# Performance work log

Measured on AMD Instinct MI355X. Metric: run time of the kernel, lower is better.

## Reference

```python
import jax, jax.numpy as jnp
import numpy as np

N_E = 8192
E_DIM = 256
BETA = 0.25
DECAY = 0.99
EPSILON = 1e-05


def setup_inputs() -> dict:
    key = jax.random.key(0)
    k1, k2 = jax.random.split(key)
    z = jax.random.normal(k1, (16, 2048, E_DIM), dtype=jnp.float32)
    # xavier_uniform for [n_e, e_dim]
    bound = float(np.sqrt(6.0 / (N_E + E_DIM)))
    embeddings = jax.random.uniform(k2, (N_E, E_DIM), dtype=jnp.float32,
                                    minval=-bound, maxval=bound)
    return {"z": z, "embeddings": embeddings}


def reference(z, embeddings):
    old_shape = z.shape
    z_flat = z.reshape(-1, E_DIM)  # [N, D]

    # squared-distance: ||z||^2 + ||e||^2 - 2 z.e  -> [N, n_e]
    distances = (jnp.sum(z_flat * z_flat, axis=1, keepdims=True)
                 + jnp.sum(embeddings * embeddings, axis=1)
                 - 2.0 * jnp.einsum('nd,kd->nk', z_flat, embeddings))
    idx = jnp.argmin(distances, axis=1)  # [N] int

    z_q = embeddings[idx].reshape(old_shape)

    # --- EMA codebook update (training, first step: counter 0 -> 1,
    # hidden starts at 0 so the bias-corrected average equals the value) ---
    ones = jnp.ones_like(idx, dtype=jnp.float32)
    bins = jax.ops.segment_sum(ones, idx, num_segments=N_E)          # [n_e]
    dw = jax.ops.segment_sum(z_flat, idx, num_segments=N_E)          # [n_e, D]
    ema_cluster = bins   # EMA step 1 with zero-init hidden == value
    ema_dw = dw
    n = jnp.sum(ema_cluster)
    cluster = (ema_cluster + EPSILON) / (n + N_E * EPSILON) * n
    new_embeddings = ema_dw / cluster[:, None]

    loss = BETA * jnp.mean((z - jax.lax.stop_gradient(z_q)) ** 2)
    z_q_st = z + jax.lax.stop_gradient(z_q - z)  # straight-through
    return z_q_st, idx, loss, new_embeddings
```

## Files before the change

kernel.cpp:

```cpp
#include <hip/hip_runtime.h>
#include <math.h>
#include <float.h>

#define N_ROWS 32768
#define EDIM 256
#define NE 8192
#define NTILES 64
#define DELTA 1.6e-3f
#define RB 8

typedef unsigned int uint32;
typedef unsigned long long uint64;
typedef __attribute__((ext_vector_type(8))) _Float16 f16x8;
typedef __attribute__((ext_vector_type(4))) float f32x4;

#define OFF_ZCAT    ((size_t)0)
#define OFF_ECAT    ((size_t)33554432)
#define OFF_ET      ((size_t)37748736)
#define OFF_EN      ((size_t)46268416)
#define OFF_PV      ((size_t)46301184)
#define OFF_PI      ((size_t)54689792)
#define OFF_PV2     ((size_t)63078400)
#define OFF_IDX     ((size_t)71467008)
#define OFF_BINS    ((size_t)71598080)
#define OFF_PACKED  ((size_t)71630848)
#define OFF_FLAGCNT ((size_t)71892992)
#define OFF_FLAGGED ((size_t)71893504)

__device__ __forceinline__ uint32 pack2_f16(float a, float b) {
    _Float16 ha = (_Float16)a;
    _Float16 hb = (_Float16)b;
    unsigned short ua = __builtin_bit_cast(unsigned short, ha);
    unsigned short ub = __builtin_bit_cast(unsigned short, hb);
    return (uint32)ua | ((uint32)ub << 16);
}

__device__ __forceinline__ void gload_lds16(const void* g, void* l) {
    __builtin_amdgcn_global_load_lds(
        (const __attribute__((address_space(1))) uint32*)g,
        (__attribute__((address_space(3))) uint32*)l, 16, 0, 0);
}

__device__ __forceinline__ float np_pairwise_sumsq(const float* a) {
#pragma clang fp contract(off)
    float h0, h1;
    #pragma unroll 1
    for (int hb = 0; hb < 2; ++hb) {
        const float* p = a + hb * 128;
        float r0=p[0]*p[0], r1=p[1]*p[1], r2=p[2]*p[2], r3=p[3]*p[3],
              r4=p[4]*p[4], r5=p[5]*p[5], r6=p[6]*p[6], r7=p[7]*p[7];
        #pragma unroll 1
        for (int i = 8; i < 128; i += 8) {
            r0 += p[i+0]*p[i+0]; r1 += p[i+1]*p[i+1];
            r2 += p[i+2]*p[i+2]; r3 += p[i+3]*p[i+3];
            r4 += p[i+4]*p[i+4]; r5 += p[i+5]*p[i+5];
            r6 += p[i+6]*p[i+6]; r7 += p[i+7]*p[i+7];
        }
        float s = ((r0+r1)+(r2+r3))+((r4+r5)+(r6+r7));
        if (hb == 0) h0 = s; else h1 = s;
    }
    return h0 + h1;
}

__global__ void k_prep(const float* __restrict__ Z, const float* __restrict__ E,
                       unsigned short* __restrict__ Zcat, unsigned short* __restrict__ Ecat,
                       float* __restrict__ ET, float* __restrict__ en,
                       uint64* __restrict__ packed, int* __restrict__ hist,
                       int* __restrict__ flagcnt) {
    __shared__ float tile[8][264];
    int b = blockIdx.x;
    int t = threadIdx.x;
    if (b < 4096) {
        int r = b * 8 + (t >> 5);
        int u = t & 31;
        int c = u >> 2, q = u & 3;
        int lq = q ^ ((r >> 1) & 3);
        int k0 = c * 32 + lq * 8;
        const float4* zp = (const float4*)(Z + (size_t)r * EDIM + k0);
        float4 a = zp[0], bb = zp[1];
        float f[8] = {a.x,a.y,a.z,a.w,bb.x,bb.y,bb.z,bb.w};
        uint32 o[4];
        #pragma unroll
        for (int j = 0; j < 4; ++j) o[j] = pack2_f16(f[2*j], f[2*j+1]);
        *(uint4*)(Zcat + (size_t)r * 256 + c * 32 + q * 8) = make_uint4(o[0],o[1],o[2],o[3]);
    } else if (b < 5120) {
        int eb = b - 4096;
        int r8 = t >> 5;
        int r = eb * 8 + r8;
        int u = t & 31;
        int c = u >> 2, q = u & 3;
        int lq = q ^ ((r >> 1) & 3);
        int k0 = c * 32 + lq * 8;
        const float4* ep = (const float4*)(E + (size_t)r * EDIM + k0);
        float4 a = ep[0], bb = ep[1];
        float f[8] = {a.x,a.y,a.z,a.w,bb.x,bb.y,bb.z,bb.w};
        uint32 o[4];
        #pragma unroll
        for (int j = 0; j < 4; ++j) o[j] = pack2_f16(256.0f*f[2*j], 256.0f*f[2*j+1]);
        *(uint4*)(Ecat + (size_t)r * 256 + c * 32 + q * 8) = make_uint4(o[0],o[1],o[2],o[3]);
        *(float4*)&tile[r8][k0]     = make_float4(f[0], f[1], f[2], f[3]);
        *(float4*)&tile[r8][k0 + 4] = make_float4(f[4], f[5], f[6], f[7]);
        __syncthreads();
        float4 lo, hi;
        lo.x = tile[0][t]; lo.y = tile[1][t]; lo.z = tile[2][t]; lo.w = tile[3][t];
        hi.x = tile[4][t]; hi.y = tile[5][t]; hi.z = tile[6][t]; hi.w = tile[7][t];
        float* dst = ET + (size_t)t * NE + eb * 8;
        *(float4*)dst = lo;
        *(float4*)(dst + 4) = hi;
    } else if (b < 5152) {
        int k = (b - 5120) * 256 + t;
        en[k] = np_pairwise_sumsq(E + (size_t)k * EDIM);
    } else if (b < 5184) {
        int i = (b - 5152) * 256 + t;
        #pragma unroll
        for (int j = 0; j < 4; ++j) packed[i + j*8192] = 0xFFFFFFFFFFFFFFFFull;
    } else {
        hist[(b - 5184) * 256 + t] = 0;
        if (b == 5184 && t == 0) *flagcnt = 0;
    }
}

__device__ __forceinline__ uint32 float_key(float v) {
    uint32 b = __float_as_uint(v);
    return (b & 0x80000000u) ? ~b : (b | 0x80000000u);
}

__global__ __launch_bounds__(256, 4) void k_gemm(
    const unsigned short* __restrict__ Zcat, const unsigned short* __restrict__ Ecat,
    const float* __restrict__ enorm,
    float* __restrict__ pv, int* __restrict__ pi, float* __restrict__ pv2)
{
    __shared__ __align__(16) char UB[33024];
    __shared__ float ens[128];
    __shared__ float fv1[128]; __shared__ int fi1[128]; __shared__ float fv2[128];

    unsigned short* As0 = (unsigned short*)(UB);
    unsigned short* As1 = (unsigned short*)(UB + 8192);
    unsigned short* Bs0 = (unsigned short*)(UB + 16384);
    unsigned short* Bs1 = (unsigned short*)(UB + 24576);

    int t = threadIdx.x;
    int nt = blockIdx.x & 63, mt = blockIdx.x >> 6;
    int wid = t >> 6, lane = t & 63;
    int wmg = wid >> 1, wng = wid & 1;
    int wm = wmg * 64, wn = wng * 64;

    if (t < 128) ens[t] = enorm[nt*128 + t];

    int j0 = wid*2, j1 = j0 + 1;
    int r0 = j0*16 + (lane >> 2), r1 = j1*16 + (lane >> 2);
    int c8 = (lane & 3) * 8;
    const unsigned short* gA0 = Zcat + (size_t)(mt*128 + r0)*256 + c8;
    const unsigned short* gA1 = Zcat + (size_t)(mt*128 + r1)*256 + c8;
    const unsigned short* gB0 = Ecat + (size_t)(nt*128 + r0)*256 + c8;
    const unsigned short* gB1 = Ecat + (size_t)(nt*128 + r1)*256 + c8;
    unsigned short* lA0s0 = As0 + j0*512;  unsigned short* lA1s0 = As0 + j1*512;
    unsigned short* lA0s1 = As1 + j0*512;  unsigned short* lA1s1 = As1 + j1*512;
    unsigned short* lB0s0 = Bs0 + j0*512;  unsigned short* lB1s0 = Bs0 + j1*512;
    unsigned short* lB0s1 = Bs1 + j0*512;  unsigned short* lB1s1 = Bs1 + j1*512;

    f32x4 acc[4][4];
    #pragma unroll
    for (int i = 0; i < 4; ++i)
        #pragma unroll
        for (int j = 0; j < 4; ++j) acc[i][j] = (f32x4){0.f,0.f,0.f,0.f};

    int frow = lane & 15, q = lane >> 4;
    int sw = (frow >> 1) & 3;
    const unsigned short* a0Base = As0 + (wm + frow)*32 + ((q ^ sw) * 8);
    const unsigned short* a1Base = As1 + (wm + frow)*32 + ((q ^ sw) * 8);
    const unsigned short* b0Base = Bs0 + (wn + frow)*32 + ((q ^ sw) * 8);
    const unsigned short* b1Base = Bs1 + (wn + frow)*32 + ((q ^ sw) * 8);

    gload_lds16(gA0, lA0s0);
    gload_lds16(gA1, lA1s0);
    gload_lds16(gB0, lB0s0);
    gload_lds16(gB1, lB1s0);
    __syncthreads();

    #pragma unroll 1
    for (int c = 0; c < 8; ++c) {
        int nxt = c + 1;
        if (nxt < 8) {
            int aOff = nxt * 32;
            if (nxt & 1) {
                gload_lds16(gA0 + aOff, lA0s1);
                gload_lds16(gA1 + aOff, lA1s1);
                gload_lds16(gB0 + aOff, lB0s1);
                gload_lds16(gB1 + aOff, lB1s1);
            } else {
                gload_lds16(gA0 + aOff, lA0s0);
                gload_lds16(gA1 + aOff, lA1s0);
                gload_lds16(gB0 + aOff, lB0s0);
                gload_lds16(gB1 + aOff, lB1s0);
            }
        }
        const unsigned short* aB = (c & 1) ? a1Base : a0Base;
        const unsigned short* bB = (c & 1) ? b1Base : b0Base;
        f16x8 af[4], bfr[4];
        #pragma unroll
        for (int i = 0; i < 4; ++i) bfr[i] = *(const f16x8*)(bB + i*16*32);
        #pragma unroll
        for (int i = 0; i < 4; ++i) af[i] = *(const f16x8*)(aB + i*16*32);
        #pragma unroll
        for (int i = 0; i < 4; ++i)
            #pragma unroll
            for (int j = 0; j < 4; ++j)
                acc[i][j] = __builtin_amdgcn_mfma_f32_16x16x32_f16(af[i], bfr[j], acc[i][j], 0, 0, 0);
        __syncthreads();
    }

    float ensr[4]; int nn[4];
    #pragma unroll
    for (int j = 0; j < 4; ++j) {
        int nl = wn + j*16 + frow;
        nn[j] = nt*128 + nl;
        ensr[j] = ens[nl];
    }
    uint4* P = (uint4*)UB;
    int gbase = wng*64 + wmg*32 + q*4;

    #pragma unroll
    for (int ih = 0; ih < 2; ++ih) {
        #pragma unroll
        for (int i2 = 0; i2 < 2; ++i2) {
            int i = ih*2 + i2;
            #pragma unroll
            for (int r = 0; r < 4; ++r) {
                float s0 = fmaf(-0.0078125f, acc[i][0][r], ensr[0]);
                float s1 = fmaf(-0.0078125f, acc[i][1][r], ensr[1]);
                float s2 = fmaf(-0.0078125f, acc[i][2][r], ensr[2]);
                float s3 = fmaf(-0.0078125f, acc[i][3][r], ensr[3]);
                float v1 = s0; int i1 = nn[0];
                float v2 = fmaxf(v1, s1);
                if (s1 < v1) i1 = nn[1];
                v1 = fminf(v1, s1);
                v2 = fminf(v2, fmaxf(v1, s2));
                if (s2 < v1) i1 = nn[2];
                v1 = fminf(v1, s2);
                v2 = fminf(v2, fmaxf(v1, s3));
                if (s3 < v1) i1 = nn[3];
                v1 = fminf(v1, s3);
                P[frow*129 + gbase + i2*16 + r] =
                    make_uint4(__float_as_uint(v1), (uint32)i1, __float_as_uint(v2), 0u);
            }
        }
        __syncthreads();
        if (t < 128) {
            const uint4* base = P + t;
            uint4 e0 = base[0];
            float v1 = __uint_as_float(e0.x); int i1 = (int)e0.y;
            float v2 = __uint_as_float(e0.z);
            #pragma unroll
            for (int f = 1; f < 16; ++f) {
                uint4 e = base[f*129];
                float ov1 = __uint_as_float(e.x), ov2 = __uint_as_float(e.z);
                v2 = fminf(fminf(v2, ov2), fmaxf(v1, ov1));
                if (ov1 < v1) i1 = (int)e.y;
                v1 = fminf(v1, ov1);
            }
            fv1[t] = v1; fi1[t] = i1; fv2[t] = v2;
        }
        __syncthreads();
        if (t < 64) {
            float v1 = fv1[t], v2 = fv2[t]; int i1 = fi1[t];
            float ov1 = fv1[64+t], ov2 = fv2[64+t];
            v2 = fminf(fminf(v2, ov2), fmaxf(v1, ov1));
            if (ov1 < v1) i1 = fi1[64+t];
            v1 = fminf(v1, ov1);
            size_t o = (size_t)nt * N_ROWS + mt*128 + (t>>5)*64 + ih*32 + (t&31);
            pv[o] = v1; pi[o] = i1; pv2[o] = v2;
        }
    }
}

__global__ void k_merge(const float* __restrict__ pv, const int* __restrict__ pi,
                        const float* __restrict__ pv2,
                        float* __restrict__ out_idx_f, int* __restrict__ idxint,
                        int* __restrict__ flagcnt, int* __restrict__ flagged) {
    int g = blockIdx.x * 256 + threadIdx.x;
    float B1 = FLT_MAX, B2 = FLT_MAX; int I1 = 0;
    #pragma unroll 1
    for (int p = 0; p < NTILES; ++p) {
        size_t o = (size_t)p * N_ROWS + g;
        float v1 = pv[o], v2 = pv2[o]; int i1 = pi[o];
        if (v1 < B1) { B2 = fminf(B1, v2); B1 = v1; I1 = i1; }
        else B2 = fminf(B2, v1);
    }
    out_idx_f[g] = (float)I1;
    idxint[g] = I1;
    if (B2 - B1 < DELTA) {
        int slot = atomicAdd(flagcnt, 1);
        flagged[slot] = g;
    }
}

__global__ void k_phaseB(const float* __restrict__ Z, const float* __restrict__ ET,
                         const float* __restrict__ enorm,
                         const int* __restrict__ flagcnt, const int* __restrict__ flagged,
                         uint64* __restrict__ packed) {
    __shared__ float zl[RB][256];
    __shared__ float znl[RB];
    __shared__ int rows[RB];
    __shared__ float sv[256]; __shared__ int si[256];
    int t = threadIdx.x;
    int cnt = *flagcnt; if (cnt > N_ROWS) cnt = N_ROWS;
    int ngrp = (cnt + RB - 1) / RB;
    int ntask = ngrp * 8;
    #pragma unroll 1
    for (int task = blockIdx.x; task < ntask; task += gridDim.x) {
        int slice = task & 7;
        int g0 = (task >> 3) * RB;
        __syncthreads();
        if (t < RB) {
            int f = g0 + t;
            rows[t] = flagged[f < cnt ? f : g0];
        }
        __syncthreads();
        #pragma unroll
        for (int rr = 0; rr < RB; ++rr) zl[rr][t] = Z[(size_t)rows[rr]*EDIM + t];
        __syncthreads();
        if (t < RB) znl[t] = np_pairwise_sumsq(&zl[t][0]);
        __syncthreads();

        float acc[RB][4];
        #pragma unroll
        for (int rr = 0; rr < RB; ++rr)
            #pragma unroll
            for (int c = 0; c < 4; ++c) acc[rr][c] = 0.f;
        const float* eb = ET + slice*1024 + t;
        #pragma unroll 1
        for (int d = 0; d < 256; ++d) {
            const float* ep = eb + (size_t)d * NE;
            float v0 = ep[0], v1 = ep[256], v2 = ep[512], v3 = ep[768];
            #pragma unroll
            for (int rr = 0; rr < RB; ++rr) {
                float zd = zl[rr][d];
                acc[rr][0] = fmaf(zd, v0, acc[rr][0]);
                acc[rr][1] = fmaf(zd, v1, acc[rr][1]);
                acc[rr][2] = fmaf(zd, v2, acc[rr][2]);
                acc[rr][3] = fmaf(zd, v3, acc[rr][3]);
            }
        }
        #pragma unroll 1
        for (int rr = 0; rr < RB; ++rr) {
            int row = rows[rr];
            float zn = znl[rr];
            float bv = FLT_MAX; int bi = 0x7fffffff;
            {
#pragma clang fp contract(off)
                #pragma unroll
                for (int c = 0; c < 4; ++c) {
                    int k = slice*1024 + c*256 + t;
                    float S  = zn + enorm[k];
                    float tw = 2.0f * acc[rr][c];
                    float sc = S - tw;
                    if (sc < bv || (sc == bv && k < bi)) { bv = sc; bi = k; }
                }
            }
            sv[t] = bv; si[t] = bi;
            __syncthreads();
            for (int st = 128; st > 0; st >>= 1) {
                if (t < st) {
                    float ov = sv[t+st]; int oi = si[t+st];
                    if (ov < sv[t] || (ov == sv[t] && oi < si[t])) { sv[t] = ov; si[t] = oi; }
                }
                __syncthreads();
            }
            if (t == 0) {
                uint64 pk = ((uint64)float_key(sv[0]) << 32) | (uint32)si[0];
                atomicMin(packed + row, pk);
            }
            __syncthreads();
        }
    }
}

__global__ void k_taila(const float* __restrict__ Z, const float* __restrict__ E,
                        int* __restrict__ idxint, const uint64* __restrict__ packed,
                        float* __restrict__ out0, float* __restrict__ out_idx_f,
                        int* __restrict__ hist, float* __restrict__ lossp) {
    __shared__ float wsum[4];
    int t = threadIdx.x;
    int w = t >> 6, lane = t & 63;
    int row = blockIdx.x * 4 + w;
    int idx = idxint[row];
    uint64 pk = packed[row];
    if (pk != 0xFFFFFFFFFFFFFFFFull) {
        idx = (int)(uint32)(pk & 0xffffffffu);
        if (lane == 0) { out_idx_f[row] = (float)idx; idxint[row] = idx; }
    }
    float4 z4 = ((const float4*)Z)[(size_t)row * 64 + lane];
    float4 e4 = ((const float4*)E)[(size_t)idx * 64 + lane];
    float4 d4; d4.x = e4.x - z4.x; d4.y = e4.y - z4.y; d4.z = e4.z - z4.z; d4.w = e4.w - z4.w;
    float4 o;  o.x = z4.x + d4.x;  o.y = z4.y + d4.y;  o.z = z4.z + d4.z;  o.w = z4.w + d4.w;
    ((float4*)out0)[(size_t)row * 64 + lane] = o;
    float q2 = d4.x*d4.x + d4.y*d4.y + d4.z*d4.z + d4.w*d4.w;
    #pragma unroll
    for (int off = 32; off > 0; off >>= 1) q2 += __shfl_down(q2, off, 64);
    if (lane == 0) { wsum[w] = q2; atomicAdd(&hist[idx], 1); }
    __syncthreads();
    if (t == 0) lossp[blockIdx.x] = wsum[0] + wsum[1] + wsum[2] + wsum[3];
}

__global__ void k_scan(const int* __restrict__ hist,
                       int* __restrict__ cursor, int* __restrict__ offs) {
    __shared__ int part[256];
    int t = threadIdx.x;
    int loc[32];
    int s = 0;
    #pragma unroll
    for (int j = 0; j < 32; ++j) { loc[j] = s; s += hist[t*32 + j]; }
    part[t] = s;
    __syncthreads();
    #pragma unroll
    for (int off = 1; off < 256; off <<= 1) {
        int u = (t >= off) ? part[t - off] : 0;
        __syncthreads();
        part[t] += u;
        __syncthreads();
    }
    int base = part[t] - s;
    #pragma unroll
    for (int j = 0; j < 32; ++j) {
        int o = base + loc[j];
        offs[t*32 + j] = o;
        cursor[t*32 + j] = o;
    }
}

__global__ void k_tailb(const int* __restrict__ idxint,
                        int* __restrict__ cursor, int* __restrict__ rowlist) {
    int g = blockIdx.x * 256 + threadIdx.x;
    int idx = idxint[g];
    int pos = atomicAdd(&cursor[idx], 1);
    rowlist[pos] = g;
}

__global__ void k_dw(const float* __restrict__ Z, const int* __restrict__ hist,
                     const int* __restrict__ offs, const int* __restrict__ rowlist,
                     const float* __restrict__ lossp,
                     float* __restrict__ out3, float* __restrict__ out2) {
    __shared__ double red[256];
    int k = blockIdx.x;
    int t = threadIdx.x;
    int cnt = hist[k];
    int start = offs[k];
    float s0 = 0.f, s1 = 0.f;
    int j = 0;
    #pragma unroll 1
    for (; j + 1 < cnt; j += 2) {
        int ra = rowlist[start + j];
        int rb = rowlist[start + j + 1];
        s0 += Z[(size_t)ra * EDIM + t];
        s1 += Z[(size_t)rb * EDIM + t];
    }
    if (j < cnt) s0 += Z[(size_t)rowlist[start + j] * EDIM + t];
    float sum = s0 + s1;
    float cl = ((float)cnt + 1e-5f) / (32768.0f + 8192.0f * 1e-5f) * 32768.0f;
    out3[(size_t)k * EDIM + t] = sum / cl;
    if (k == 0) {
        double s = 0.0;
        #pragma unroll 1
        for (int p = t; p < 8192; p += 256) s += (double)lossp[p];
        red[t] = s;
        __syncthreads();
        #pragma unroll
        for (int st = 128; st > 0; st >>= 1) {
            if (t < st) red[t] += red[t + st];
            __syncthreads();
        }
        if (t == 0) out2[0] = 0.25f * (float)(red[0] / 8388608.0);
    }
}

extern "C" void kernel_launch(void* const* d_in, const int* in_sizes, int n_in,
                              void* d_out, int out_size, void* d_ws, size_t ws_size,
                              hipStream_t stream) {
    const float* Z = (const float*)d_in[0];
    const float* E = (const float*)d_in[1];
    float* out  = (float*)d_out;
    float* out0 = out;
    float* out1 = out + 8388608;
    float* out2 = out1 + 32768;
    float* out3 = out2 + 1;

    char* ws = (char*)d_ws;
    unsigned short* Zcat = (unsigned short*)(ws + OFF_ZCAT);
    unsigned short* Ecat = (unsigned short*)(ws + OFF_ECAT);
    float*  ET      = (float*)(ws + OFF_ET);
    float*  enorm   = (float*)(ws + OFF_EN);
    float*  pv      = (float*)(ws + OFF_PV);
    int*    pi      = (int*)  (ws + OFF_PI);
    float*  pv2     = (float*)(ws + OFF_PV2);
    int*    idxint  = (int*)  (ws + OFF_IDX);
    int*    hist    = (int*)  (ws + OFF_BINS);
    uint64* packed  = (uint64*)(ws + OFF_PACKED);
    int*    flagcnt = (int*)  (ws + OFF_FLAGCNT);
    int*    flagged = (int*)  (ws + OFF_FLAGGED);
    float*  lossp   = (float*)(ws + OFF_PV);
    int*    rowlist = (int*)  (ws + OFF_PV + 32768);
    int*    cursor  = (int*)  (ws + OFF_PV2);
    int*    offs    = (int*)  (ws + OFF_PV2 + 32768);

    k_prep   <<<5216,         256, 0, stream>>>(Z, E, Zcat, Ecat, ET, enorm,
                                                packed, hist, flagcnt);
    k_gemm   <<<256 * NTILES, 256, 0, stream>>>(Zcat, Ecat, enorm, pv, pi, pv2);
    k_merge  <<<N_ROWS / 256, 256, 0, stream>>>(pv, pi, pv2, out1, idxint, flagcnt, flagged);
    k_phaseB <<<2048,         256, 0, stream>>>(Z, ET, enorm, flagcnt, flagged, packed);
    k_taila  <<<N_ROWS / 4,   256, 0, stream>>>(Z, E, idxint, packed, out0, out1, hist, lossp);
    k_scan   <<<1,            256, 0, stream>>>(hist, cursor, offs);
    k_tailb  <<<N_ROWS / 256, 256, 0, stream>>>(idxint, cursor, rowlist);
    k_dw     <<<NE,           256, 0, stream>>>(Z, hist, offs, rowlist, lossp, out3, out2);
}
```

Measured before the change: 436.6 us.

## Triple-buffer GEMM LDS staging with explicit waitcnt and fuse codebook norms into prep

The GEMM main loop goes from double-buffered LDS loads with a full __syncthreads per K-chunk to a fully unrolled three-stage pipeline. It uses hand-placed vmcnt waits and raw s_barrier so two global-to-LDS loads stay in flight while one chunk is computed. Separately, the codebook squared norms are now computed from the already-staged transpose tile inside k_prep, which drops the separate norm blocks that re-read E from global memory. LDS per block grows from about 33KB to 49KB, which may reduce occupancy. The manual waitcnt counts must match the number of outstanding loads.

```diff
diff --git a/kernel.cpp b/kernel.cpp
--- a/kernel.cpp
+++ b/kernel.cpp
@@ -107,16 +107,14 @@
         float* dst = ET + (size_t)t * NE + eb * 8;
         *(float4*)dst = lo;
         *(float4*)(dst + 4) = hi;
+        if (t < 8) en[eb * 8 + t] = np_pairwise_sumsq(&tile[t][0]);
     } else if (b < 5152) {
-        int k = (b - 5120) * 256 + t;
-        en[k] = np_pairwise_sumsq(E + (size_t)k * EDIM);
-    } else if (b < 5184) {
-        int i = (b - 5152) * 256 + t;
+        int i = (b - 5120) * 256 + t;
         #pragma unroll
         for (int j = 0; j < 4; ++j) packed[i + j*8192] = 0xFFFFFFFFFFFFFFFFull;
     } else {
-        hist[(b - 5184) * 256 + t] = 0;
-        if (b == 5184 && t == 0) *flagcnt = 0;
+        hist[(b - 5152) * 256 + t] = 0;
+        if (b == 5152 && t == 0) *flagcnt = 0;
     }
 }
 
@@ -130,14 +128,16 @@
     const float* __restrict__ enorm,
     float* __restrict__ pv, int* __restrict__ pi, float* __restrict__ pv2)
 {
-    __shared__ __align__(16) char UB[33024];
+    __shared__ __align__(16) char UB[49152];
     __shared__ float ens[128];
     __shared__ float fv1[128]; __shared__ int fi1[128]; __shared__ float fv2[128];
 
     unsigned short* As0 = (unsigned short*)(UB);
     unsigned short* As1 = (unsigned short*)(UB + 8192);
-    unsigned short* Bs0 = (unsigned short*)(UB + 16384);
-    unsigned short* Bs1 = (unsigned short*)(UB + 24576);
+    unsigned short* As2 = (unsigned short*)(UB + 16384);
+    unsigned short* Bs0 = (unsigned short*)(UB + 24576);
+    unsigned short* Bs1 = (unsigned short*)(UB + 32768);
+    unsigned short* Bs2 = (unsigned short*)(UB + 40960);
 
     int t = threadIdx.x;
     int nt = blockIdx.x & 63, mt = blockIdx.x >> 6;
@@ -154,10 +154,6 @@
     const unsigned short* gA1 = Zcat + (size_t)(mt*128 + r1)*256 + c8;
     const unsigned short* gB0 = Ecat + (size_t)(nt*128 + r0)*256 + c8;
     const unsigned short* gB1 = Ecat + (size_t)(nt*128 + r1)*256 + c8;
-    unsigned short* lA0s0 = As0 + j0*512;  unsigned short* lA1s0 = As0 + j1*512;
-    unsigned short* lA0s1 = As1 + j0*512;  unsigned short* lA1s1 = As1 + j1*512;
-    unsigned short* lB0s0 = Bs0 + j0*512;  unsigned short* lB1s0 = Bs0 + j1*512;
-    unsigned short* lB0s1 = Bs1 + j0*512;  unsigned short* lB1s1 = Bs1 + j1*512;
 
     f32x4 acc[4][4];
     #pragma unroll
@@ -167,48 +163,67 @@
 
     int frow = lane & 15, q = lane >> 4;
     int sw = (frow >> 1) & 3;
-    const unsigned short* a0Base = As0 + (wm + frow)*32 + ((q ^ sw) * 8);
-    const unsigned short* a1Base = As1 + (wm + frow)*32 + ((q ^ sw) * 8);
-    const unsigned short* b0Base = Bs0 + (wn + frow)*32 + ((q ^ sw) * 8);
-    const unsigned short* b1Base = Bs1 + (wn + frow)*32 + ((q ^ sw) * 8);
-
-    gload_lds16(gA0, lA0s0);
-    gload_lds16(gA1, lA1s0);
-    gload_lds16(gB0, lB0s0);
-    gload_lds16(gB1, lB1s0);
+    int aoffs = (wm + frow)*32 + ((q ^ sw) * 8);
+    int boffs = (wn + frow)*32 + ((q ^ sw) * 8);
+    const unsigned short* a0Base = As0 + aoffs;
+    const unsigned short* a1Base = As1 + aoffs;
+    const unsigned short* a2Base = As2 + aoffs;
+    const unsigned short* b0Base = Bs0 + boffs;
+    const unsigned short* b1Base = Bs1 + boffs;
+    const unsigned short* b2Base = Bs2 + boffs;
+
+#define STAGE(cc, AS, BS) do { \
+    gload_lds16(gA0 + (cc)*32, (AS) + j0*512); \
+    gload_lds16(gA1 + (cc)*32, (AS) + j1*512); \
+    gload_lds16(gB0 + (cc)*32, (BS) + j0*512); \
+    gload_lds16(gB1 + (cc)*32, (BS) + j1*512); \
+} while (0)
+
+#define COMPUTE(aB, bB) do { \
+    f16x8 af_[4], bf_[4]; \
+    _Pragma("unroll") \
+    for (int i_ = 0; i_ < 4; ++i_) bf_[i_] = *(const f16x8*)((bB) + i_*16*32); \
+    _Pragma("unroll") \
+    for (int i_ = 0; i_ < 4; ++i_) af_[i_] = *(const f16x8*)((aB) + i_*16*32); \
+    _Pragma("unroll") \
+    for (int i_ = 0; i_ < 4; ++i_) \
+        _Pragma("unroll") \
+        for (int j_ = 0; j_ < 4; ++j_) \
+            acc[i_][j_] = __builtin_amdgcn_mfma_f32_16x16x32_f16(af_[i_], bf_[j_], acc[i_][j_], 0, 0, 0); \
+} while (0)
+
+#define PHASE_WAIT do { \
+    asm volatile("s_waitcnt vmcnt(4) lgkmcnt(0)" ::: "memory"); \
+    __builtin_amdgcn_sched_barrier(0); \
+    __builtin_amdgcn_s_barrier(); \
+    __builtin_amdgcn_sched_barrier(0); \
+} while (0)
+
+#define FINAL_WAIT do { \
+    asm volatile("s_waitcnt vmcnt(0) lgkmcnt(0)" ::: "memory"); \
+    __builtin_amdgcn_sched_barrier(0); \
+    __builtin_amdgcn_s_barrier(); \
+    __builtin_amdgcn_sched_barrier(0); \
+} while (0)
+
+    STAGE(0, As0, Bs0);
+    STAGE(1, As1, Bs1);
+
+    PHASE_WAIT; STAGE(2, As2, Bs2); COMPUTE(a0Base, b0Base);
+    PHASE_WAIT; STAGE(3, As0, Bs0); COMPUTE(a1Base, b1Base);
+    PHASE_WAIT; STAGE(4, As1, Bs1); COMPUTE(a2Base, b2Base);
+    PHASE_WAIT; STAGE(5, As2, Bs2); COMPUTE(a0Base, b0Base);
+    PHASE_WAIT; STAGE(6, As0, Bs0); COMPUTE(a1Base, b1Base);
+    PHASE_WAIT; STAGE(7, As1, Bs1); COMPUTE(a2Base, b2Base);
+    PHASE_WAIT;                     COMPUTE(a0Base, b0Base);
+    FINAL_WAIT;                     COMPUTE(a1Base, b1Base);
+
     __syncthreads();
 
-    #pragma unroll 1
-    for (int c = 0; c < 8; ++c) {
-        int nxt = c + 1;
-        if (nxt < 8) {
-            int aOff = nxt * 32;
-            if (nxt & 1) {
-                gload_lds16(gA0 + aOff, lA0s1);
-                gload_lds16(gA1 + aOff, lA1s1);
-                gload_lds16(gB0 + aOff, lB0s1);
-                gload_lds16(gB1 + aOff, lB1s1);
-            } else {
-                gload_lds16(gA0 + aOff, lA0s0);
-                gload_lds16(gA1 + aOff, lA1s0);
-                gload_lds16(gB0 + aOff, lB0s0);
-                gload_lds16(gB1 + aOff, lB1s0);
-            }
-        }
-        const unsigned short* aB = (c & 1) ? a1Base : a0Base;
-        const unsigned short* bB = (c & 1) ? b1Base : b0Base;
-        f16x8 af[4], bfr[4];
-        #pragma unroll
-        for (int i = 0; i < 4; ++i) bfr[i] = *(const f16x8*)(bB + i*16*32);
-        #pragma unroll
-        for (int i = 0; i < 4; ++i) af[i] = *(const f16x8*)(aB + i*16*32);
-        #pragma unroll
-        for (int i = 0; i < 4; ++i)
-            #pragma unroll
-            for (int j = 0; j < 4; ++j)
-                acc[i][j] = __builtin_amdgcn_mfma_f32_16x16x32_f16(af[i], bfr[j], acc[i][j], 0, 0, 0);
-        __syncthreads();
-    }
+#undef STAGE
+#undef COMPUTE
+#undef PHASE_WAIT
+#undef FINAL_WAIT
 
     float ensr[4]; int nn[4];
     #pragma unroll
@@ -503,7 +518,7 @@
     int*    cursor  = (int*)  (ws + OFF_PV2);
     int*    offs    = (int*)  (ws + OFF_PV2 + 32768);
 
-    k_prep   <<<5216,         256, 0, stream>>>(Z, E, Zcat, Ecat, ET, enorm,
+    k_prep   <<<5184,         256, 0, stream>>>(Z, E, Zcat, Ecat, ET, enorm,
                                                 packed, hist, flagcnt);
     k_gemm   <<<256 * NTILES, 256, 0, stream>>>(Zcat, Ecat, enorm, pv, pi, pv2);
     k_merge  <<<N_ROWS / 256, 256, 0, stream>>>(pv, pi, pv2, out1, idxint, flagcnt, flagged);
```

Measured after the change: 438.9 us. Within noise of the previous version (+0.5%).
